# Kernel tuning notes

Measured on AMD Instinct MI355X. Metric: run time of the kernel, lower is better.

Reference implementation:

```python
import jax, jax.numpy as jnp
import numpy as np

MAX_ITER = 3  # module default init kwarg
B, S = 16, 128


def setup_inputs() -> dict:
    key = jax.random.key(0)
    k1, k2, k3 = jax.random.split(key, 3)
    s_span = jax.random.normal(k1, (B, S, S), dtype=jnp.float32)
    s_pair = jax.random.normal(k2, (B, S, S, S), dtype=jnp.float32)
    mask = jax.random.randint(k3, (B, S, S), 0, 2).astype(jnp.bool_)
    return {"s_span": s_span, "s_pair": s_pair, "mask": mask}


def reference(s_span, s_pair, mask):
    # Faithful batch-first translation of MFVIConstituency.mfvi + sigmoid.
    # torch code works in [S, S, B] layout; here we keep [B, S, S].
    seq_len = mask.shape[1]
    idx = jnp.arange(seq_len)
    # ls[i,j]=min(i,j), rs[i,j]=max(i,j) (stack(where(ones)).sort(0) trick)
    ls = jnp.minimum(idx[:, None], idx[None, :])  # [S, S]
    rs = jnp.maximum(idx[:, None], idx[None, :])  # [S, S]
    # exclude k == min(i,j) and k == max(i,j): [S, S, S] over (i, j, k)
    ne = (ls[:, :, None] != idx[None, None, :]) & (rs[:, :, None] != idx[None, None, :])
    # span_mask broadcast in torch aligns trailing dims -> indexed at (j, k):
    # mask2o[b,i,j,k] &= mask[b,k,j] | mask[b,j,k]
    span = mask | jnp.swapaxes(mask, 1, 2)  # [B, S, S] symmetric
    # mask2o[b,i,j,k] = mask[b,i,j] & ne[i,j,k] & span[b,j,k]
    mask2o = mask[:, :, :, None] & ne[None, :, :, :] & span[:, None, :, :]
    sp = s_pair * mask2o.astype(s_pair.dtype)  # [B, S, S, S]
    q = s_span
    for _ in range(MAX_ITER):
        q = jax.nn.sigmoid(q)
        # q_new[b,i,j] = s_span[b,i,j] + sum_k q[b,i,k] * sp[b,i,j,k]
        q = s_span + jnp.einsum('bik,bijk->bij', q, sp)
    return jax.nn.sigmoid(q)  # marginals [B, S, S]
```

## Files before the change

kernel.cpp:

```cpp
#include <hip/hip_runtime.h>
#include <hip/hip_bf16.h>


#define S 128
#define MB_STRIDE 132

static __device__ __forceinline__ float fsig(float x) {
    return __builtin_amdgcn_rcpf(1.0f + __expf(-x));
}

__global__ __launch_bounds__(256, 2) void pack_masks(
    const int* __restrict__ mask,
    unsigned* __restrict__ spanw,
    unsigned char* __restrict__ actg,
    int* __restrict__ nactg)
{
    __shared__ unsigned char mb[S * MB_STRIDE];
    const int t = threadIdx.x, b = blockIdx.x;
    const int* mrow = mask + (long long)b * (S * S);
    #pragma unroll
    for (int s2 = 0; s2 < 16; ++s2) {
        int f4 = t + 256 * s2;
        int j  = f4 >> 5;
        int k0 = (f4 & 31) * 4;
        int4 v = *(const int4*)(mrow + f4 * 4);
        unsigned packed = (v.x ? 1u : 0u)
                        | ((v.y ? 1u : 0u) << 8)
                        | ((v.z ? 1u : 0u) << 16)
                        | ((v.w ? 1u : 0u) << 24);
        *(unsigned*)(mb + j * MB_STRIDE + k0) = packed;
    }
    __syncthreads();

    #pragma unroll
    for (int r = 0; r < 2; ++r) {
        int task = t * 2 + r;
        int j = task >> 2, w = task & 3;
        unsigned sbits = 0;
        #pragma unroll
        for (int c = 0; c < 32; ++c) {
            int k = w * 32 + c;
            sbits |= ((mb[j * MB_STRIDE + k] | mb[k * MB_STRIDE + j]) ? 1u : 0u) << c;
        }
        spanw[(b * S + j) * 4 + w] = sbits;
    }

    {
        int wave = t >> 6, lane = t & 63;
        for (int r = 0; r < 32; ++r) {
            int i = wave * 32 + r;
            unsigned char* dst = actg + (long long)(b * S + i) * S;
            bool a0 = mb[i * MB_STRIDE + lane] != 0;
            unsigned long long b0 = __ballot(a0);
            int n0 = __popcll(b0);
            if (a0) dst[__popcll(b0 & ((1ull << lane) - 1ull))] = (unsigned char)lane;
            bool a1 = mb[i * MB_STRIDE + 64 + lane] != 0;
            unsigned long long b1 = __ballot(a1);
            if (a1) dst[n0 + __popcll(b1 & ((1ull << lane) - 1ull))] = (unsigned char)(64 + lane);
            if (lane == 0) nactg[b * S + i] = n0 + __popcll(b1);
        }
    }
}

__global__ __launch_bounds__(256, 4) void mfvi_main(
    const float* __restrict__ s_span,
    const float* __restrict__ s_pair,
    const int* __restrict__ mask,
    const unsigned* __restrict__ spanw,
    const unsigned char* __restrict__ actg,
    const int* __restrict__ nactg,
    float* __restrict__ out)
{
    __shared__ unsigned      sw_l[S * 4];
    __shared__ float         prow2[2][S];
    __shared__ float         qsv [S];
    __shared__ unsigned char act_l[S];

    const int t  = threadIdx.x;
    const int bi = blockIdx.x;
    const int i  = bi & (S - 1);
    const int b  = bi >> 7;
    const int row0 = t >> 5;
    const int L    = t & 31;
    const int c4   = L * 4;
    const float* tile = s_pair + (long long)bi * (S * S);
    float* outrow = out + (long long)bi * S;
    const int nact = nactg[bi];

    if (t < S) {
        act_l[t] = actg[(long long)bi * S + t];
        *(uint4*)&sw_l[t * 4] = *(const uint4*)&spanw[(b * S + t) * 4];
        float sv = s_span[(long long)bi * S + t];
        qsv[t] = sv;
        float p0 = fsig(sv);
        prow2[0][t] = p0;
        prow2[1][t] = p0;
        if (!mask[(long long)bi * S + t])
            outrow[t] = p0;
    }
    __syncthreads();

    float4 v[16];
    #pragma unroll
    for (int s = 0; s < 16; ++s) {
        int idx = row0 + 8 * s;
        if (idx < nact) {
            int j = act_l[idx];
            float4 x = *(const float4*)(tile + j * S + c4);
            unsigned cw = sw_l[j * 4 + (c4 >> 5)];
            int lo = i < j ? i : j, hi = i < j ? j : i;
            if ((lo >> 5) == (c4 >> 5)) cw &= ~(1u << (lo & 31));
            if ((hi >> 5) == (c4 >> 5)) cw &= ~(1u << (hi & 31));
            unsigned cs = cw >> (c4 & 31);
            x.x = __int_as_float(__float_as_int(x.x) & (((int)(cs << 31)) >> 31));
            x.y = __int_as_float(__float_as_int(x.y) & (((int)(cs << 30)) >> 31));
            x.z = __int_as_float(__float_as_int(x.z) & (((int)(cs << 29)) >> 31));
            x.w = __int_as_float(__float_as_int(x.w) & (((int)(cs << 28)) >> 31));
            v[s] = x;
        } else {
            v[s] = make_float4(0.f, 0.f, 0.f, 0.f);
        }
    }

    #pragma unroll
    for (int it = 0; it < 3; ++it) {
        const float* pr = prow2[it & 1];
        float*       pw = prow2[(it + 1) & 1];
        float4 p = *(const float4*)&pr[c4];
        float acc[16];
        #pragma unroll
        for (int s = 0; s < 16; ++s)
            acc[s] = v[s].x * p.x + v[s].y * p.y + v[s].z * p.z + v[s].w * p.w;

        #pragma unroll
        for (int m = 0; m < 8; ++m) {
            float a = acc[2 * m], bb = acc[2 * m + 1];
            float sent = (L & 1) ? a : bb;
            float keep = (L & 1) ? bb : a;
            acc[m] = keep + __shfl_xor(sent, 1);
        }
        #pragma unroll
        for (int m = 0; m < 4; ++m) {
            float a = acc[2 * m], bb = acc[2 * m + 1];
            float sent = (L & 2) ? a : bb;
            float keep = (L & 2) ? bb : a;
            acc[m] = keep + __shfl_xor(sent, 2);
        }
        #pragma unroll
        for (int m = 0; m < 2; ++m) {
            float a = acc[2 * m], bb = acc[2 * m + 1];
            float sent = (L & 4) ? a : bb;
            float keep = (L & 4) ? bb : a;
            acc[m] = keep + __shfl_xor(sent, 4);
        }
        float r;
        {
            float a = acc[0], bb = acc[1];
            float sent = (L & 8) ? a : bb;
            float keep = (L & 8) ? bb : a;
            r = keep + __shfl_xor(sent, 8);
        }
        r += __shfl_xor(r, 16);

        if (L < 16) {
            int idx = row0 + 8 * L;
            if (idx < nact) {
                int j = act_l[idx];
                float q = qsv[j] + r;
                if (it < 2) pw[j] = fsig(q);
                else        outrow[j] = fsig(q);
            }
        }
        if (it < 2) __syncthreads();
    }
}

extern "C" void kernel_launch(void* const* d_in, const int* in_sizes, int n_in,
                              void* d_out, int out_size, void* d_ws, size_t ws_size,
                              hipStream_t stream) {
    const float* s_span = (const float*)d_in[0];
    const float* s_pair = (const float*)d_in[1];
    const int*   mask   = (const int*)d_in[2];
    float*       out    = (float*)d_out;

    int num_rows = in_sizes[0] / S;
    int B        = in_sizes[2] / (S * S);

    unsigned*      ws_span = (unsigned*)d_ws;
    unsigned char* ws_act  = (unsigned char*)(ws_span + (size_t)B * S * 4);
    int*           ws_nact = (int*)(ws_act + (size_t)B * S * S);

    pack_masks<<<B, 256, 0, stream>>>(mask, ws_span, ws_act, ws_nact);
    mfvi_main<<<num_rows, 256, 0, stream>>>(s_span, s_pair, mask,
                                            ws_span, ws_act, ws_nact, out);
}
```

Measured before the change: 199.0 us.

## Drop compacted active-row lists; use row mask bits and prefolded span exclusions

Removes the ballot-based compaction of active rows in pack_masks and the per-row active index lists. The main kernel now walks rows in their natural order and gates each row load with a bitmask built from the mask row. The diagonal exclusions are folded into the span words ahead of time, once in pack_masks and once per block, so the inner loop no longer does per-element lo/hi bit clearing. This removes a serial loop and workspace traffic from the pack kernel, but masked rows are no longer packed together, so wavefronts can end up with uneven amounts of work.

```diff
diff --git a/kernel.cpp b/kernel.cpp
--- a/kernel.cpp
+++ b/kernel.cpp
@@ -11,9 +11,7 @@
 
 __global__ __launch_bounds__(256, 2) void pack_masks(
     const int* __restrict__ mask,
-    unsigned* __restrict__ spanw,
-    unsigned char* __restrict__ actg,
-    int* __restrict__ nactg)
+    unsigned* __restrict__ spanw)
 {
     __shared__ unsigned char mb[S * MB_STRIDE];
     const int t = threadIdx.x, b = blockIdx.x;
@@ -42,23 +40,8 @@
             int k = w * 32 + c;
             sbits |= ((mb[j * MB_STRIDE + k] | mb[k * MB_STRIDE + j]) ? 1u : 0u) << c;
         }
+        if ((j >> 5) == w) sbits &= ~(1u << (j & 31));
         spanw[(b * S + j) * 4 + w] = sbits;
-    }
-
-    {
-        int wave = t >> 6, lane = t & 63;
-        for (int r = 0; r < 32; ++r) {
-            int i = wave * 32 + r;
-            unsigned char* dst = actg + (long long)(b * S + i) * S;
-            bool a0 = mb[i * MB_STRIDE + lane] != 0;
-            unsigned long long b0 = __ballot(a0);
-            int n0 = __popcll(b0);
-            if (a0) dst[__popcll(b0 & ((1ull << lane) - 1ull))] = (unsigned char)lane;
-            bool a1 = mb[i * MB_STRIDE + 64 + lane] != 0;
-            unsigned long long b1 = __ballot(a1);
-            if (a1) dst[n0 + __popcll(b1 & ((1ull << lane) - 1ull))] = (unsigned char)(64 + lane);
-            if (lane == 0) nactg[b * S + i] = n0 + __popcll(b1);
-        }
     }
 }
 
@@ -67,14 +50,12 @@
     const float* __restrict__ s_pair,
     const int* __restrict__ mask,
     const unsigned* __restrict__ spanw,
-    const unsigned char* __restrict__ actg,
-    const int* __restrict__ nactg,
     float* __restrict__ out)
 {
-    __shared__ unsigned      sw_l[S * 4];
-    __shared__ float         prow2[2][S];
-    __shared__ float         qsv [S];
-    __shared__ unsigned char act_l[S];
+    __shared__ unsigned sw_l[S * 4];
+    __shared__ float    prow2[2][S];
+    __shared__ float    qsv [S];
+    __shared__ int      mrow_l[S];
 
     const int t  = threadIdx.x;
     const int bi = blockIdx.x;
@@ -85,40 +66,38 @@
     const int c4   = L * 4;
     const float* tile = s_pair + (long long)bi * (S * S);
     float* outrow = out + (long long)bi * S;
-    const int nact = nactg[bi];
 
     if (t < S) {
-        act_l[t] = actg[(long long)bi * S + t];
-        *(uint4*)&sw_l[t * 4] = *(const uint4*)&spanw[(b * S + t) * 4];
+        uint4 sw = *(const uint4*)&spanw[(b * S + t) * 4];
+        ((unsigned*)&sw)[i >> 5] &= ~(1u << (i & 31));
+        *(uint4*)&sw_l[t * 4] = sw;
+        mrow_l[t] = mask[(long long)bi * S + t];
         float sv = s_span[(long long)bi * S + t];
         qsv[t] = sv;
         float p0 = fsig(sv);
         prow2[0][t] = p0;
         prow2[1][t] = p0;
-        if (!mask[(long long)bi * S + t])
-            outrow[t] = p0;
     }
     __syncthreads();
+
+    unsigned rowbits = 0;
+    #pragma unroll
+    for (int s = 0; s < 16; ++s)
+        rowbits |= (mrow_l[row0 + 8 * s] ? 1u : 0u) << s;
 
     float4 v[16];
     #pragma unroll
     for (int s = 0; s < 16; ++s) {
-        int idx = row0 + 8 * s;
-        if (idx < nact) {
-            int j = act_l[idx];
+        v[s] = make_float4(0.f, 0.f, 0.f, 0.f);
+        if (rowbits & (1u << s)) {
+            int j = row0 + 8 * s;
             float4 x = *(const float4*)(tile + j * S + c4);
-            unsigned cw = sw_l[j * 4 + (c4 >> 5)];
-            int lo = i < j ? i : j, hi = i < j ? j : i;
-            if ((lo >> 5) == (c4 >> 5)) cw &= ~(1u << (lo & 31));
-            if ((hi >> 5) == (c4 >> 5)) cw &= ~(1u << (hi & 31));
-            unsigned cs = cw >> (c4 & 31);
+            unsigned cs = sw_l[j * 4 + (L >> 3)] >> (c4 & 31);
             x.x = __int_as_float(__float_as_int(x.x) & (((int)(cs << 31)) >> 31));
             x.y = __int_as_float(__float_as_int(x.y) & (((int)(cs << 30)) >> 31));
             x.z = __int_as_float(__float_as_int(x.z) & (((int)(cs << 29)) >> 31));
             x.w = __int_as_float(__float_as_int(x.w) & (((int)(cs << 28)) >> 31));
             v[s] = x;
-        } else {
-            v[s] = make_float4(0.f, 0.f, 0.f, 0.f);
         }
     }
 
@@ -163,13 +142,10 @@
         r += __shfl_xor(r, 16);
 
         if (L < 16) {
-            int idx = row0 + 8 * L;
-            if (idx < nact) {
-                int j = act_l[idx];
-                float q = qsv[j] + r;
-                if (it < 2) pw[j] = fsig(q);
-                else        outrow[j] = fsig(q);
-            }
+            int j = row0 + 8 * L;
+            float q = qsv[j] + r;
+            if (it < 2) pw[j] = fsig(q);
+            else        outrow[j] = fsig(q);
         }
         if (it < 2) __syncthreads();
     }
@@ -186,11 +162,8 @@
     int num_rows = in_sizes[0] / S;
     int B        = in_sizes[2] / (S * S);
 
-    unsigned*      ws_span = (unsigned*)d_ws;
-    unsigned char* ws_act  = (unsigned char*)(ws_span + (size_t)B * S * 4);
-    int*           ws_nact = (int*)(ws_act + (size_t)B * S * S);
+    unsigned* ws_span = (unsigned*)d_ws;
 
-    pack_masks<<<B, 256, 0, stream>>>(mask, ws_span, ws_act, ws_nact);
-    mfvi_main<<<num_rows, 256, 0, stream>>>(s_span, s_pair, mask,
-                                            ws_span, ws_act, ws_nact, out);
+    pack_masks<<<B, 256, 0, stream>>>(mask, ws_span);
+    mfvi_main<<<num_rows, 256, 0, stream>>>(s_span, s_pair, mask, ws_span, out);
 }
```

New measurement: 203.5 us. 2.3% more time.
